# Kernel optimization log

Measured on AMD Instinct MI355X. Metric: run time of the kernel, lower is better.

## Reference

```python
import jax, jax.numpy as jnp
import numpy as np

ROPE_THETA = 10000.0

def _apply_rope(x, theta=ROPE_THETA):
    # x: [B, H, L, d_head]
    L, d_k = x.shape[-2], x.shape[-1]
    inv_freq = 1.0 / (theta ** (jnp.arange(0, d_k, 2, dtype=jnp.float32) / d_k))  # [d_k/2]
    ang = jnp.arange(L, dtype=jnp.float32)[:, None] * inv_freq[None, :]           # [L, d_k/2]
    ang = jnp.repeat(ang, 2, axis=-1)                                             # [L, d_k] interleaved
    xr = x.reshape(x.shape[:-1] + (d_k // 2, 2))
    rot = jnp.stack((-xr[..., 1], xr[..., 0]), axis=-1).reshape(x.shape)
    return x * jnp.cos(ang) + rot * jnp.sin(ang)

def setup_inputs() -> dict:
    key = jax.random.key(0)
    k1, k2, k3 = jax.random.split(key, 3)
    B, L, D = 2, 2048, 2048
    std_qkv = np.sqrt(2.0 / (D + 3 * D)).astype(np.float32)
    std_o = np.sqrt(2.0 / (D + D)).astype(np.float32)
    return {
        "x": jax.random.normal(k1, (B, L, D), dtype=jnp.float32),
        "W_qkv": jax.random.normal(k2, (3 * D, D), dtype=jnp.float32) * std_qkv,
        "W_o": jax.random.normal(k3, (D, D), dtype=jnp.float32) * std_o,
    }

def reference(x, W_qkv, W_o):
    B, L, D = x.shape
    H = 16
    dh = D // H
    qkv = jnp.einsum('bld,ed->ble', x, W_qkv)            # [B, L, 3D]
    q, k, v = jnp.split(qkv, 3, axis=-1)
    # [B, H, L, dh]
    q = q.reshape(B, L, H, dh).transpose(0, 2, 1, 3)
    k = k.reshape(B, L, H, dh).transpose(0, 2, 1, 3)
    v = v.reshape(B, L, H, dh).transpose(0, 2, 1, 3)
    q = _apply_rope(q)
    k = _apply_rope(k)
    scale = 1.0 / np.sqrt(dh).astype(np.float32)
    att = jnp.einsum('bhqd,bhkd->bhqk', q, k) * scale    # [B, H, L, L]
    causal = jnp.tril(jnp.ones((L, L), dtype=bool))
    att = jnp.where(causal, att, -jnp.inf)
    p = jax.nn.softmax(att, axis=-1)
    y = jnp.einsum('bhqk,bhkd->bhqd', p, v)              # [B, H, L, dh]
    y = y.transpose(0, 2, 1, 3).reshape(B, L, D)
    return jnp.einsum('bld,ed->ble', y, W_o)
```

## Files before the change

### kernel.cpp

```cpp
#include <hip/hip_runtime.h>
#include <math.h>

typedef __bf16 bf16x8 __attribute__((ext_vector_type(8)));
typedef float f32x4 __attribute__((ext_vector_type(4)));
typedef unsigned short us8 __attribute__((ext_vector_type(8)));

#define B_ 2
#define L_ 2048
#define D_ 2048
#define H_ 16
#define DH 128

__device__ __forceinline__ unsigned short f2b(float f) {
  union { float f; unsigned u; } v; v.f = f;
  unsigned u = v.u;
  return (unsigned short)((u + 0x7fffu + ((u >> 16) & 1u)) >> 16);
}
__device__ __forceinline__ float b2f(unsigned short h) {
  union { unsigned u; float f; } v; v.u = ((unsigned)h) << 16;
  return v.f;
}

#define GLD16(g, l) __builtin_amdgcn_global_load_lds(                          \
    (const __attribute__((address_space(1))) void*)(g),                        \
    (__attribute__((address_space(3))) void*)(l), 16, 0, 0)

#define SBAR() __builtin_amdgcn_s_barrier()
#define LGK0() asm volatile("s_waitcnt lgkmcnt(0)")
#define VMC6() asm volatile("s_waitcnt vmcnt(6)" ::: "memory")
#define VMC0() asm volatile("s_waitcnt vmcnt(0)" ::: "memory")

__global__ void f32_to_bf16(const float* __restrict__ in,
                            unsigned short* __restrict__ out, int n4) {
  int i = blockIdx.x * blockDim.x + threadIdx.x;
  const int stride = gridDim.x * blockDim.x;
  for (; i < n4; i += stride) {
    const float4 v = ((const float4*)in)[i];
    ushort4 o;
    o.x = f2b(v.x); o.y = f2b(v.y); o.z = f2b(v.z); o.w = f2b(v.w);
    ((ushort4*)out)[i] = o;
  }
}

template <bool OUT_BF16>
__global__ __launch_bounds__(512)
void gemm3b(const unsigned short* __restrict__ A,
            const unsigned short* __restrict__ Bm,
            void* __restrict__ Cv, int M, int N, int K) {
  __shared__ __align__(16) unsigned short lA[3][128 * 64];
  __shared__ __align__(16) unsigned short lB[3][2][128 * 64];
  const int tid = threadIdx.x;
  const int w = tid >> 6, lane = tid & 63;
  const int lo = lane & 15, hi = lane >> 4;
  const int mh = w >> 2;
  const int wn = (w & 3) * 64;
  const int bhalf = wn >> 7;
  const int brb = (wn & 64) + lo;
  const int GM = M >> 7;
  const int nwg = gridDim.x;
  const int f = blockIdx.x;
  const int v = (f & 7) * (nwg >> 3) + (f >> 3);
  const int bn = v / GM, bm = v % GM;
  const int NT = K >> 6;

  const int row64 = tid >> 3;
  const int gs = (tid & 7) ^ (row64 & 7);
  auto stA = [&](int buf, int u, int tile) {
    GLD16(A + (long)(bm * 128 + u * 64 + row64) * K + tile * 64 + gs * 8,
          &lA[buf][u * 4096 + (tid & ~63) * 8]);
  };
  auto stB = [&](int buf, int hf, int u, int tile) {
    GLD16(Bm + (long)(bn * 256 + hf * 128 + u * 64 + row64) * K + tile * 64 + gs * 8,
          &lB[buf][hf][u * 4096 + (tid & ~63) * 8]);
  };

  f32x4 acc[4][4] = {};

  stA(0, 0, 0); stA(0, 1, 0);
  stB(0, 0, 0, 0); stB(0, 0, 1, 0); stB(0, 1, 0, 0); stB(0, 1, 1, 0);
  stA(1, 0, 1); stA(1, 1, 1);
  stB(1, 0, 0, 1); stB(1, 0, 1, 1); stB(1, 1, 0, 1); stB(1, 1, 1, 1);
  VMC6();
  SBAR();

  for (int t = 0; t < NT; ++t) {
    const int bt = t % 3;
    const int b2 = (t + 2) % 3;
    const bool nx = (t + 2 < NT);
    bf16x8 af[4], bf[4];
#pragma unroll
    for (int mi = 0; mi < 4; ++mi) {
      const int r = mh * 64 + mi * 16 + lo;
      af[mi] = *(const bf16x8*)&lA[bt][r * 64 + ((hi ^ (r & 7)) * 8)];
    }
#pragma unroll
    for (int ni = 0; ni < 4; ++ni) {
      const int rb = brb + ni * 16;
      bf[ni] = *(const bf16x8*)&lB[bt][bhalf][rb * 64 + ((hi ^ (rb & 7)) * 8)];
    }
    if (nx) { stA(b2, 0, t + 2); stA(b2, 1, t + 2); stB(b2, 0, 0, t + 2); }
    SBAR(); LGK0();
    __builtin_amdgcn_s_setprio(1);
#pragma unroll
    for (int mi = 0; mi < 4; ++mi)
#pragma unroll
      for (int ni = 0; ni < 4; ++ni)
        acc[mi][ni] = __builtin_amdgcn_mfma_f32_16x16x32_bf16(
            af[mi], bf[ni], acc[mi][ni], 0, 0, 0);
    __builtin_amdgcn_s_setprio(0);
#pragma unroll
    for (int mi = 0; mi < 4; ++mi) {
      const int r = mh * 64 + mi * 16 + lo;
      af[mi] = *(const bf16x8*)&lA[bt][r * 64 + (((4 + hi) ^ (r & 7)) * 8)];
    }
#pragma unroll
    for (int ni = 0; ni < 4; ++ni) {
      const int rb = brb + ni * 16;
      bf[ni] = *(const bf16x8*)&lB[bt][bhalf][rb * 64 + (((4 + hi) ^ (rb & 7)) * 8)];
    }
    if (nx) { stB(b2, 0, 1, t + 2); stB(b2, 1, 0, t + 2); stB(b2, 1, 1, t + 2); }
    SBAR(); LGK0();
    __builtin_amdgcn_s_setprio(1);
#pragma unroll
    for (int mi = 0; mi < 4; ++mi)
#pragma unroll
      for (int ni = 0; ni < 4; ++ni)
        acc[mi][ni] = __builtin_amdgcn_mfma_f32_16x16x32_bf16(
            af[mi], bf[ni], acc[mi][ni], 0, 0, 0);
    __builtin_amdgcn_s_setprio(0);
    if (t < NT - 2) VMC6(); else VMC0();
    SBAR();
  }

  const int r0 = bm * 128 + mh * 64;
  const int c0 = bn * 256 + wn;
#pragma unroll
  for (int mi = 0; mi < 4; ++mi) {
#pragma unroll
    for (int r = 0; r < 4; ++r) {
      const long row = r0 + mi * 16 + hi * 4 + r;
#pragma unroll
      for (int ni = 0; ni < 4; ++ni) {
        const int col = c0 + ni * 16 + lo;
        if (OUT_BF16)
          ((unsigned short*)Cv)[row * N + col] = f2b(acc[mi][ni][r]);
        else
          ((float*)Cv)[row * N + col] = acc[mi][ni][r];
      }
    }
  }
}

__global__ void rope_qk(const unsigned short* __restrict__ qkv,
                        unsigned short* __restrict__ Qo,
                        unsigned short* __restrict__ Ko) {
  const int idx = blockIdx.x * 256 + threadIdx.x;
  const int i = idx & 63;
  const int l = (idx >> 6) & (L_ - 1);
  const int h = (idx >> 17) & (H_ - 1);
  const int b = idx >> 21;
  const float invf = exp2f(-(float)i * 0.20762050593045077f);
  const float ang = (float)l * invf;
  float sn, cs;
  sincosf(ang, &sn, &cs);
  const long base = ((long)b * L_ + l) * (3 * D_) + h * DH + 2 * i;
  const unsigned qin = *(const unsigned*)&qkv[base];
  const unsigned kin = *(const unsigned*)&qkv[base + D_];
  const float q0 = b2f((unsigned short)qin), q1 = b2f((unsigned short)(qin >> 16));
  const float k0 = b2f((unsigned short)kin), k1 = b2f((unsigned short)(kin >> 16));
  const float sc = 0.12751743f;
  const float qo0 = (q0 * cs - q1 * sn) * sc, qo1 = (q1 * cs + q0 * sn) * sc;
  const float ko0 = (k0 * cs - k1 * sn), ko1 = (k1 * cs + k0 * sn);
  const long oo = ((long)(b * H_ + h) * L_ + l) * DH + 2 * i;
  *(unsigned*)&Qo[oo] = (unsigned)f2b(qo0) | ((unsigned)f2b(qo1) << 16);
  *(unsigned*)&Ko[oo] = (unsigned)f2b(ko0) | ((unsigned)f2b(ko1) << 16);
}

__global__ __launch_bounds__(256)
void v_fragpack(const unsigned short* __restrict__ qkv,
                unsigned short* __restrict__ Vf) {
  const int lblk = blockIdx.x;
  const int bh = blockIdx.y;
  const int b = bh >> 4, h = bh & 15;
  __shared__ unsigned short tile[64 * 137];
  const int tid = threadIdx.x;
  const int l0 = lblk * 64;
#pragma unroll
  for (int j = 0; j < 4; ++j) {
    const int c = j * 256 + tid;
    const int row = c >> 4, col8 = c & 15;
    const us8 v = *(const us8*)&qkv[((long)b * L_ + l0 + row) * (3 * D_) +
                                    2 * D_ + h * DH + col8 * 8];
    unsigned short* dst = &tile[row * 137 + col8 * 8];
#pragma unroll
    for (int e = 0; e < 8; ++e) dst[e] = v[e];
  }
  __syncthreads();
#pragma unroll
  for (int j = 0; j < 4; ++j) {
    const int c = j * 256 + tid;
    const int k32l = c >> 9, t2 = (c >> 6) & 7, lane = c & 63;
    const int lo = lane & 15, hi = lane >> 4;
    us8 v;
#pragma unroll
    for (int e = 0; e < 8; ++e)
      v[e] = tile[(k32l * 32 + hi * 8 + e) * 137 + t2 * 16 + lo];
    *(us8*)&Vf[(((size_t)bh * 64 + lblk * 2 + k32l) * 8 + t2) * 512 + lane * 8] = v;
  }
}

__global__ __launch_bounds__(256, 2)
void flash_attn3(const unsigned short* __restrict__ Q,
                 const unsigned short* __restrict__ Kg,
                 const unsigned short* __restrict__ Vf,
                 unsigned short* __restrict__ Y) {
  const int p = blockIdx.x;
  const int tA = p, tB = (L_ / 64 - 1) - p;
  const int h = blockIdx.y, b = blockIdx.z;
  const int tid = threadIdx.x;
  const int wave = tid >> 6, lane = tid & 63;
  const int lo = lane & 15, hi = lane >> 4;
  const int swz = (lo & 7) << 4;
  const int qA = tA * 64 + wave * 16;
  const int qB = tB * 64 + wave * 16;
  const long hoff = ((long)(b * H_ + h)) * L_ * DH;
  const unsigned short* Qh = Q + hoff;
  const unsigned short* Kh = Kg + hoff;
  const unsigned short* Vfh = Vf + ((size_t)(b * H_ + h)) * (64 * 8 * 512);

  __shared__ unsigned short lK[2][64 * 128];
  __shared__ unsigned short pl[4][2][16 * 72];
  unsigned short* plA = &pl[wave][0][0];
  unsigned short* plB = &pl[wave][1][0];

  auto stage = [&](int bufi, int kv0s) {
    unsigned short* bk = &lK[bufi][0];
#pragma unroll
    for (int j = 0; j < 4; ++j) {
      const int c = j * 256 + tid;
      const int row = c >> 4;
      const int soff = ((c & 15) ^ (row & 7)) << 3;
      GLD16(Kh + (long)(kv0s + row) * DH + soff, &bk[(c & ~63) * 8]);
    }
  };

  bf16x8 qfA[4], qfB[4];
#pragma unroll
  for (int s = 0; s < 4; ++s) {
    qfA[s] = *(const bf16x8*)&Qh[(long)(qA + lo) * DH + s * 32 + hi * 8];
    qfB[s] = *(const bf16x8*)&Qh[(long)(qB + lo) * DH + s * 32 + hi * 8];
  }

  float mA = -INFINITY, lsA = 0.f, mB = -INFINITY, lsB = 0.f;
  f32x4 yA[8] = {}, yB[8] = {};

  auto softmax = [&](f32x4 (&st)[4], float& m, float& lsum, f32x4 (&yacc)[8],
                     unsigned short* plw, int qw, int kv0) {
    if (kv0 + 63 > qw) {
      const int d0 = qw + lo - kv0 - hi * 4;
#pragma unroll
      for (int t = 0; t < 4; ++t) {
        const int dt = d0 - t * 16;
#pragma unroll
        for (int r = 0; r < 4; ++r)
          if (r > dt) st[t][r] = -INFINITY;
      }
    }
    float tm0 = fmaxf(fmaxf(st[0][0], st[0][1]), fmaxf(st[0][2], st[0][3]));
    float tm1 = fmaxf(fmaxf(st[1][0], st[1][1]), fmaxf(st[1][2], st[1][3]));
    float tm2 = fmaxf(fmaxf(st[2][0], st[2][1]), fmaxf(st[2][2], st[2][3]));
    float tm3 = fmaxf(fmaxf(st[3][0], st[3][1]), fmaxf(st[3][2], st[3][3]));
    float rm = fmaxf(fmaxf(tm0, tm1), fmaxf(tm2, tm3));
    rm = fmaxf(rm, __shfl_xor(rm, 16));
    rm = fmaxf(rm, __shfl_xor(rm, 32));
    if (!__all(rm <= m + 8.f)) {
      const float mn = fmaxf(m, rm);
      const float alpha = exp2f(m - mn);
      m = mn;
      lsum *= alpha;
      float ar[4];
#pragma unroll
      for (int r = 0; r < 4; ++r) ar[r] = __shfl(alpha, hi * 4 + r);
#pragma unroll
      for (int t2 = 0; t2 < 8; ++t2)
#pragma unroll
        for (int r = 0; r < 4; ++r) yacc[t2][r] *= ar[r];
    }
    float rs = 0.f;
#pragma unroll
    for (int t = 0; t < 4; ++t) {
#pragma unroll
      for (int r2 = 0; r2 < 2; ++r2) {
        const float e0 = exp2f(st[t][2 * r2] - m);
        const float e1 = exp2f(st[t][2 * r2 + 1] - m);
        rs += e0 + e1;
        const unsigned short u0 = __builtin_bit_cast(unsigned short, (__bf16)e0);
        const unsigned short u1 = __builtin_bit_cast(unsigned short, (__bf16)e1);
        *(unsigned*)&plw[lo * 72 + t * 16 + hi * 4 + 2 * r2] =
            (unsigned)u0 | ((unsigned)u1 << 16);
      }
    }
    rs += __shfl_xor(rs, 16);
    rs += __shfl_xor(rs, 32);
    lsum += rs;
  };

  const int nIter = tB + 1;
  stage(0, 0);
  __syncthreads();

  for (int it = 0; it < nIter; ++it) {
    const int kv0 = it * 64;
    const bool aAct = (it <= tA);
    if (it + 1 < nIter) stage((it + 1) & 1, kv0 + 64);
    const char* bkc = (const char*)&lK[it & 1][0];
    f32x4 stA[4] = {}, stB[4] = {};
    if (aAct) {
#pragma unroll
      for (int s = 0; s < 4; ++s) {
        const int inner = (lo * 256 + s * 64 + hi * 16) ^ swz;
#pragma unroll
        for (int t = 0; t < 4; ++t) {
          const bf16x8 kf = *(const bf16x8*)(bkc + t * 4096 + inner);
          stA[t] = __builtin_amdgcn_mfma_f32_16x16x32_bf16(kf, qfA[s], stA[t], 0, 0, 0);
          stB[t] = __builtin_amdgcn_mfma_f32_16x16x32_bf16(kf, qfB[s], stB[t], 0, 0, 0);
        }
      }
    } else {
#pragma unroll
      for (int s = 0; s < 4; ++s) {
        const int inner = (lo * 256 + s * 64 + hi * 16) ^ swz;
#pragma unroll
        for (int t = 0; t < 4; ++t) {
          const bf16x8 kf = *(const bf16x8*)(bkc + t * 4096 + inner);
          stB[t] = __builtin_amdgcn_mfma_f32_16x16x32_bf16(kf, qfB[s], stB[t], 0, 0, 0);
        }
      }
    }
    if (aAct) softmax(stA, mA, lsA, yA, plA, qA, kv0);
    softmax(stB, mB, lsB, yB, plB, qB, kv0);
    const unsigned short* vbase = Vfh + (size_t)(it * 16) * 512 + lane * 8;
#pragma unroll
    for (int kt = 0; kt < 2; ++kt) {
      bf16x8 vf[8];
#pragma unroll
      for (int t2 = 0; t2 < 8; ++t2)
        vf[t2] = *(const bf16x8*)(vbase + (size_t)(kt * 8 + t2) * 512);
      const bf16x8 pfB = *(const bf16x8*)&plB[lo * 72 + kt * 32 + hi * 8];
#pragma unroll
      for (int t2 = 0; t2 < 8; ++t2)
        yB[t2] = __builtin_amdgcn_mfma_f32_16x16x32_bf16(pfB, vf[t2], yB[t2], 0, 0, 0);
      if (aAct) {
        const bf16x8 pfA = *(const bf16x8*)&plA[lo * 72 + kt * 32 + hi * 8];
#pragma unroll
        for (int t2 = 0; t2 < 8; ++t2)
          yA[t2] = __builtin_amdgcn_mfma_f32_16x16x32_bf16(pfA, vf[t2], yA[t2], 0, 0, 0);
      }
    }
    __syncthreads();
  }

  auto wout = [&](f32x4 (&yacc)[8], float lsum, int qw) {
    const float inv = 1.f / lsum;
    float ir[4];
#pragma unroll
    for (int r = 0; r < 4; ++r) ir[r] = __shfl(inv, hi * 4 + r);
#pragma unroll
    for (int r = 0; r < 4; ++r) {
      const long row = qw + hi * 4 + r;
      unsigned short* yrow = Y + ((long)b * L_ + row) * D_ + h * DH;
#pragma unroll
      for (int t2 = 0; t2 < 8; ++t2)
        yrow[t2 * 16 + lo] = f2b(yacc[t2][r] * ir[r]);
    }
  };
  wout(yA, lsA, qA);
  wout(yB, lsB, qB);
}

extern "C" void kernel_launch(void* const* d_in, const int* in_sizes, int n_in,
                              void* d_out, int out_size, void* d_ws, size_t ws_size,
                              hipStream_t stream) {
  const float* x = (const float*)d_in[0];
  const float* wqkv = (const float*)d_in[1];
  const float* wo = (const float*)d_in[2];
  float* out = (float*)d_out;

  unsigned short* ws = (unsigned short*)d_ws;
  const size_t N_X = (size_t)B_ * L_ * D_;
  const size_t N_WQKV = (size_t)3 * D_ * D_;
  const size_t N_WO = (size_t)D_ * D_;
  const size_t N_QKV = (size_t)B_ * L_ * 3 * D_;
  const size_t N_HEAD = (size_t)B_ * H_ * L_ * DH;
  unsigned short* xb = ws;
  unsigned short* wqkb = xb + N_X;
  unsigned short* wob = wqkb + N_WQKV;
  unsigned short* qkv = wob + N_WO;
  unsigned short* Qb = qkv + N_QKV;
  unsigned short* Kb = Qb + N_HEAD;
  unsigned short* Vf = Kb + N_HEAD;
  unsigned short* Yb = Vf + N_HEAD;
  const size_t need = (size_t)(Yb + N_HEAD - ws) * sizeof(unsigned short);
  if (ws_size < need) return;

  f32_to_bf16<<<2048, 256, 0, stream>>>(x, xb, (int)(N_X / 4));
  f32_to_bf16<<<2048, 256, 0, stream>>>(wqkv, wqkb, (int)(N_WQKV / 4));
  f32_to_bf16<<<2048, 256, 0, stream>>>(wo, wob, (int)(N_WO / 4));

  gemm3b<true><<<(B_ * L_ / 128) * (3 * D_ / 256), 512, 0, stream>>>(
      xb, wqkb, qkv, B_ * L_, 3 * D_, D_);

  rope_qk<<<(B_ * H_ * L_ * 64) / 256, 256, 0, stream>>>(qkv, Qb, Kb);
  v_fragpack<<<dim3(L_ / 64, B_ * H_), 256, 0, stream>>>(qkv, Vf);

  flash_attn3<<<dim3(16, H_, B_), 256, 0, stream>>>(Qb, Kb, Vf, Yb);

  gemm3b<false><<<(B_ * L_ / 128) * (D_ / 256), 512, 0, stream>>>(
      Yb, wob, out, B_ * L_, D_, D_);
}
```

Before: 290.6 us.

## Shrink GEMM K-tile to 32 for higher occupancy and merge f32-to-bf16 conversion launches

The GEMM is rewritten to use a K-step of 32 instead of 64, which cuts LDS use by half. It adds launch_bounds(512,4) to raise occupancy, drops one of the two in-loop barriers, and uses inline ds_read_b128 with precomputed LDS offsets under a new swizzle. The three fp32-to-bf16 conversion kernels are merged into one launch. In exchange each iteration does half the MFMA work per barrier and wait, so sync overhead per FLOP rises, and the register cap could cause spills.

```diff
diff --git a/kernel.cpp b/kernel.cpp
--- a/kernel.cpp
+++ b/kernel.cpp
@@ -27,108 +27,113 @@
 
 #define SBAR() __builtin_amdgcn_s_barrier()
 #define LGK0() asm volatile("s_waitcnt lgkmcnt(0)")
-#define VMC6() asm volatile("s_waitcnt vmcnt(6)" ::: "memory")
+#define SCB0() __builtin_amdgcn_sched_barrier(0)
+#define VMC3() asm volatile("s_waitcnt vmcnt(3)" ::: "memory")
 #define VMC0() asm volatile("s_waitcnt vmcnt(0)" ::: "memory")
 
-__global__ void f32_to_bf16(const float* __restrict__ in,
-                            unsigned short* __restrict__ out, int n4) {
+__device__ __forceinline__ unsigned ldsoff(const void* p) {
+  return (unsigned)(unsigned long long)(const __attribute__((address_space(3))) char*)p;
+}
+__device__ __forceinline__ bf16x8 dsr128(unsigned a) {
+  bf16x8 r;
+  asm volatile("ds_read_b128 %0, %1" : "=v"(r) : "v"(a));
+  return r;
+}
+
+__global__ void f32_to_bf16_3(const float* __restrict__ a, int na4,
+                              const float* __restrict__ b, int nb4,
+                              const float* __restrict__ c, int nc4,
+                              unsigned short* __restrict__ oa,
+                              unsigned short* __restrict__ ob,
+                              unsigned short* __restrict__ oc) {
+  const int total = na4 + nb4 + nc4;
   int i = blockIdx.x * blockDim.x + threadIdx.x;
   const int stride = gridDim.x * blockDim.x;
-  for (; i < n4; i += stride) {
-    const float4 v = ((const float4*)in)[i];
+  for (; i < total; i += stride) {
+    const float* src;
+    unsigned short* dst;
+    int j = i;
+    if (j < na4) { src = a; dst = oa; }
+    else if (j < na4 + nb4) { j -= na4; src = b; dst = ob; }
+    else { j -= na4 + nb4; src = c; dst = oc; }
+    const float4 v = ((const float4*)src)[j];
     ushort4 o;
     o.x = f2b(v.x); o.y = f2b(v.y); o.z = f2b(v.z); o.w = f2b(v.w);
-    ((ushort4*)out)[i] = o;
+    ((ushort4*)dst)[j] = o;
   }
 }
 
 template <bool OUT_BF16>
-__global__ __launch_bounds__(512)
-void gemm3b(const unsigned short* __restrict__ A,
-            const unsigned short* __restrict__ Bm,
-            void* __restrict__ Cv, int M, int N, int K) {
-  __shared__ __align__(16) unsigned short lA[3][128 * 64];
-  __shared__ __align__(16) unsigned short lB[3][2][128 * 64];
+__global__ __launch_bounds__(512, 4)
+void gemmk32(const unsigned short* __restrict__ A,
+             const unsigned short* __restrict__ Bm,
+             void* __restrict__ Cv, int M, int N, int K) {
+  __shared__ __align__(16) unsigned short lA[3][128 * 32];
+  __shared__ __align__(16) unsigned short lB[3][256 * 32];
   const int tid = threadIdx.x;
   const int w = tid >> 6, lane = tid & 63;
   const int lo = lane & 15, hi = lane >> 4;
   const int mh = w >> 2;
   const int wn = (w & 3) * 64;
-  const int bhalf = wn >> 7;
-  const int brb = (wn & 64) + lo;
   const int GM = M >> 7;
   const int nwg = gridDim.x;
   const int f = blockIdx.x;
   const int v = (f & 7) * (nwg >> 3) + (f >> 3);
   const int bn = v / GM, bm = v % GM;
-  const int NT = K >> 6;
-
-  const int row64 = tid >> 3;
-  const int gs = (tid & 7) ^ (row64 & 7);
-  auto stA = [&](int buf, int u, int tile) {
-    GLD16(A + (long)(bm * 128 + u * 64 + row64) * K + tile * 64 + gs * 8,
-          &lA[buf][u * 4096 + (tid & ~63) * 8]);
+  const int NT = K >> 5;
+
+  const int srow = tid >> 2;
+  const int gs = (tid & 3) ^ ((srow >> 1) & 3);
+  auto stA = [&](int buf, int tile) {
+    GLD16(A + (long)(bm * 128 + srow) * K + tile * 32 + gs * 8,
+          &lA[buf][(tid & ~63) * 8]);
   };
-  auto stB = [&](int buf, int hf, int u, int tile) {
-    GLD16(Bm + (long)(bn * 256 + hf * 128 + u * 64 + row64) * K + tile * 64 + gs * 8,
-          &lB[buf][hf][u * 4096 + (tid & ~63) * 8]);
+  auto stB = [&](int buf, int u, int tile) {
+    GLD16(Bm + (long)(bn * 256 + u * 128 + srow) * K + tile * 32 + gs * 8,
+          &lB[buf][u * 4096 + (tid & ~63) * 8]);
   };
 
+  unsigned aoff[4], boff[4];
+#pragma unroll
+  for (int mi = 0; mi < 4; ++mi) {
+    const int r = mh * 64 + mi * 16 + lo;
+    aoff[mi] = ldsoff(&lA[0][0]) + r * 64 + ((hi ^ ((r >> 1) & 3)) * 16);
+  }
+#pragma unroll
+  for (int ni = 0; ni < 4; ++ni) {
+    const int rb = wn + ni * 16 + lo;
+    boff[ni] = ldsoff(&lB[0][0]) + rb * 64 + ((hi ^ ((rb >> 1) & 3)) * 16);
+  }
+
   f32x4 acc[4][4] = {};
 
-  stA(0, 0, 0); stA(0, 1, 0);
-  stB(0, 0, 0, 0); stB(0, 0, 1, 0); stB(0, 1, 0, 0); stB(0, 1, 1, 0);
-  stA(1, 0, 1); stA(1, 1, 1);
-  stB(1, 0, 0, 1); stB(1, 0, 1, 1); stB(1, 1, 0, 1); stB(1, 1, 1, 1);
-  VMC6();
+  stA(0, 0); stB(0, 0, 0); stB(0, 1, 0);
+  stA(1, 1); stB(1, 0, 1); stB(1, 1, 1);
+  VMC3();
   SBAR();
 
   for (int t = 0; t < NT; ++t) {
     const int bt = t % 3;
     const int b2 = (t + 2) % 3;
     const bool nx = (t + 2 < NT);
-    bf16x8 af[4], bf[4];
-#pragma unroll
-    for (int mi = 0; mi < 4; ++mi) {
-      const int r = mh * 64 + mi * 16 + lo;
-      af[mi] = *(const bf16x8*)&lA[bt][r * 64 + ((hi ^ (r & 7)) * 8)];
-    }
-#pragma unroll
-    for (int ni = 0; ni < 4; ++ni) {
-      const int rb = brb + ni * 16;
-      bf[ni] = *(const bf16x8*)&lB[bt][bhalf][rb * 64 + ((hi ^ (rb & 7)) * 8)];
-    }
-    if (nx) { stA(b2, 0, t + 2); stA(b2, 1, t + 2); stB(b2, 0, 0, t + 2); }
-    SBAR(); LGK0();
+    const unsigned ab = (unsigned)(bt * 8192);
+    const unsigned bb = (unsigned)(bt * 16384);
+    bf16x8 af[4], bfv[4];
+#pragma unroll
+    for (int mi = 0; mi < 4; ++mi) af[mi] = dsr128(aoff[mi] + ab);
+#pragma unroll
+    for (int ni = 0; ni < 4; ++ni) bfv[ni] = dsr128(boff[ni] + bb);
+    if (nx) { stA(b2, t + 2); stB(b2, 0, t + 2); stB(b2, 1, t + 2); }
+    LGK0(); SCB0();
     __builtin_amdgcn_s_setprio(1);
 #pragma unroll
     for (int mi = 0; mi < 4; ++mi)
 #pragma unroll
       for (int ni = 0; ni < 4; ++ni)
         acc[mi][ni] = __builtin_amdgcn_mfma_f32_16x16x32_bf16(
-            af[mi], bf[ni], acc[mi][ni], 0, 0, 0);
+            af[mi], bfv[ni], acc[mi][ni], 0, 0, 0);
     __builtin_amdgcn_s_setprio(0);
-#pragma unroll
-    for (int mi = 0; mi < 4; ++mi) {
-      const int r = mh * 64 + mi * 16 + lo;
-      af[mi] = *(const bf16x8*)&lA[bt][r * 64 + (((4 + hi) ^ (r & 7)) * 8)];
-    }
-#pragma unroll
-    for (int ni = 0; ni < 4; ++ni) {
-      const int rb = brb + ni * 16;
-      bf[ni] = *(const bf16x8*)&lB[bt][bhalf][rb * 64 + (((4 + hi) ^ (rb & 7)) * 8)];
-    }
-    if (nx) { stB(b2, 0, 1, t + 2); stB(b2, 1, 0, t + 2); stB(b2, 1, 1, t + 2); }
-    SBAR(); LGK0();
-    __builtin_amdgcn_s_setprio(1);
-#pragma unroll
-    for (int mi = 0; mi < 4; ++mi)
-#pragma unroll
-      for (int ni = 0; ni < 4; ++ni)
-        acc[mi][ni] = __builtin_amdgcn_mfma_f32_16x16x32_bf16(
-            af[mi], bf[ni], acc[mi][ni], 0, 0, 0);
-    __builtin_amdgcn_s_setprio(0);
-    if (t < NT - 2) VMC6(); else VMC0();
+    if (t < NT - 2) VMC3(); else VMC0();
     SBAR();
   }
 
@@ -403,11 +408,11 @@
   const size_t need = (size_t)(Yb + N_HEAD - ws) * sizeof(unsigned short);
   if (ws_size < need) return;
 
-  f32_to_bf16<<<2048, 256, 0, stream>>>(x, xb, (int)(N_X / 4));
-  f32_to_bf16<<<2048, 256, 0, stream>>>(wqkv, wqkb, (int)(N_WQKV / 4));
-  f32_to_bf16<<<2048, 256, 0, stream>>>(wo, wob, (int)(N_WO / 4));
-
-  gemm3b<true><<<(B_ * L_ / 128) * (3 * D_ / 256), 512, 0, stream>>>(
+  f32_to_bf16_3<<<2048, 256, 0, stream>>>(
+      x, (int)(N_X / 4), wqkv, (int)(N_WQKV / 4), wo, (int)(N_WO / 4),
+      xb, wqkb, wob);
+
+  gemmk32<true><<<(B_ * L_ / 128) * (3 * D_ / 256), 512, 0, stream>>>(
       xb, wqkb, qkv, B_ * L_, 3 * D_, D_);
 
   rope_qk<<<(B_ * H_ * L_ * 64) / 256, 256, 0, stream>>>(qkv, Qb, Kb);
@@ -415,6 +420,6 @@
 
   flash_attn3<<<dim3(16, H_, B_), 256, 0, stream>>>(Qb, Kb, Vf, Yb);
 
-  gemm3b<false><<<(B_ * L_ / 128) * (D_ / 256), 512, 0, stream>>>(
+  gemmk32<false><<<(B_ * L_ / 128) * (D_ / 256), 512, 0, stream>>>(
       Yb, wob, out, B_ * L_, D_, D_);
 }
```

Result: no change. 286.0 us (-1.6%).
